# Kernel optimization log

Hardware: AMD Instinct MI355X
Metric: run time of the kernel (lower is better)

Reference implementation:

```python
import jax, jax.numpy as jnp
import numpy as np

PATCH = 3  # patch_size (init kwarg)
STRIDE = 1  # stride (init kwarg)
EPS_NORMALIZE = 1e-12  # F.normalize default eps
EPS_PATCH = 1e-5       # patch-norm eps in feature_match_index


def _unit_channels(feat):
    # F.normalize(feat.reshape(c,-1), dim=0): unit L2 norm over channels per pixel.
    n = jnp.linalg.norm(feat, axis=0, keepdims=True)
    return feat / jnp.maximum(n, EPS_NORMALIZE)


def _patches(feat, ps):
    # feat: (c, h, w) -> (c*ps*ps, n_patches) row-major over (h-ps+1, w-ps+1)
    c, h, w = feat.shape
    hp, wp = h - ps + 1, w - ps + 1
    cols = jnp.stack([feat[:, dy:dy + hp, dx:dx + wp]
                      for dy in range(ps) for dx in range(ps)], axis=1)  # (c, ps*ps, hp, wp)
    return cols.reshape(c * ps * ps, hp * wp)


def _per_item(fi, fr):
    # fi, fr: (c, h, w)
    c, h, w = fi.shape
    ps = PATCH
    hp, wp = h - ps + 1, w - ps + 1

    fi = _unit_channels(fi)
    fr = _unit_channels(fr)

    ref = _patches(fr, ps)                                   # (c*9, n_ref)
    ref = ref / (jnp.linalg.norm(ref, axis=0, keepdims=True) + EPS_PATCH)
    inp = _patches(fi, ps)                                   # (c*9, n_in)

    # Full cross-correlation cost volume (= chunked conv2d + running max in torch code)
    corr = jnp.einsum('ki,kr->ir', inp, ref)                 # (n_in, n_ref)
    max_idx = jnp.argmax(corr, axis=1).reshape(hp, wp)       # first occurrence on ties, same as torch running '>' max

    # index_to_flow
    flow_w = (max_idx % wp).astype(jnp.float32)
    flow_h = (max_idx // wp).astype(jnp.float32)
    grid_x = jnp.arange(wp, dtype=jnp.float32)[None, :]
    grid_y = jnp.arange(hp, dtype=jnp.float32)[:, None]
    flow = jnp.stack([flow_w - grid_x * jnp.ones((hp, wp), jnp.float32),
                      flow_h - grid_y * jnp.ones((hp, wp), jnp.float32)], axis=-1)  # (hp, wp, 2)
    flow = jnp.pad(flow, ((0, ps - 1), (0, ps - 1), (0, 0)))  # (h, w, 2)

    # tensor_shift for (i, j) in {0,1,2}^2, zero fill
    shifted = jnp.stack([jnp.pad(flow, ((i, 0), (j, 0), (0, 0)))[:h, :w]
                         for i in range(3) for j in range(3)], axis=0)  # (9, h, w, 2)
    return shifted


def setup_inputs() -> dict:
    key = jax.random.key(0)
    k1, k2 = jax.random.split(key)
    N, C, H, W = 2, 64, 96, 96
    return {
        'dense_features1': jax.random.normal(k1, (N, C, H, W), dtype=jnp.float32),
        'dense_features2': jax.random.normal(k2, (N, C, H, W), dtype=jnp.float32),
    }


def reference(dense_features1, dense_features2):
    shifted = jax.vmap(_per_item)(dense_features1, dense_features2)  # (N, 9, H, W, 2)
    N, _, H, W, _ = shifted.shape
    # pre_offset_reorder: even channels = flow_h (offset[...,1]), odd channels = flow_w (offset[...,0])
    out = jnp.stack([shifted[..., 1], shifted[..., 0]], axis=2).reshape(N, 18, H, W)
    return out
```

## Files before the change

kernel.cpp:

```cpp
#include <hip/hip_runtime.h>
#include <math.h>

static constexpr int NITEM = 2;
static constexpr int C = 64;
static constexpr int W = 96;
static constexpr int H = 96;
static constexpr int HW = H * W;
static constexpr int HP = 94;
static constexpr int NP = HP * HP;

static constexpr int PL = 8;
static constexpr int UNITS_PER_N = 1188;
static constexpr int NBLOCKS = 768;

typedef float f32x2 __attribute__((ext_vector_type(2)));

#if defined(__has_builtin) && __has_builtin(__builtin_elementwise_fma)
#define VFMA(q, a, b) (q) = __builtin_elementwise_fma((a), (b), (q))
#else
#define VFMA(q, a, b) do { (q).x = fmaf((a).x, (b).x, (q).x); \
                           (q).y = fmaf((a).y, (b).y, (q).y); } while (0)
#endif

__device__ __forceinline__ unsigned int fkey(float v) {
    unsigned int u = __float_as_uint(v);
    return (u & 0x80000000u) ? ~u : (u | 0x80000000u);
}

__global__ __launch_bounds__(256) void normalize_kernel(
    const float* __restrict__ f1, const float* __restrict__ f2,
    float2* __restrict__ fiP, float* __restrict__ frP, float* __restrict__ ssn)
{
    int t = blockIdx.x * 256 + threadIdx.x;
    const int perTensor = NITEM * HW;
    if (t >= 2 * perTensor) return;
    int which = t / perTensor;
    int p = t - which * perTensor;
    int n = p / HW;
    int pix = p - n * HW;
    const float* src = (which ? f2 : f1) + (size_t)n * C * HW + pix;
    float s = 0.f;
    #pragma unroll
    for (int c = 0; c < C; c++) {
        float v = src[c * HW];
        s = fmaf(v, v, s);
    }
    float norm = sqrtf(s);
    float scale = 1.0f / fmaxf(norm, 1e-12f);
    int y = pix / W, x = pix - y * W;
    if (which) {
        float* base = frP + ((size_t)n * H + y) * (C * W) + x;
        #pragma unroll
        for (int c = 0; c < C; c++)
            base[c * W] = src[c * HW] * scale;
        ssn[p] = s * scale * scale;
    } else {
        float2* base = fiP + ((size_t)n * H + y) * (32 * W) + x;
        #pragma unroll
        for (int c2 = 0; c2 < 32; c2++)
            base[c2 * W] = make_float2(src[(2 * c2) * HW] * scale,
                                       src[(2 * c2 + 1) * HW] * scale);
    }
}

__global__ __launch_bounds__(256) void refnorm_kernel(
    const float* __restrict__ ssn, float* __restrict__ invn)
{
    int t = blockIdx.x * 256 + threadIdx.x;
    if (t >= NITEM * NP) return;
    int n = t / NP;
    int r = t - n * NP;
    int yr = r / HP, xr = r - yr * HP;
    const float* s = ssn + n * HW;
    float acc = 0.f;
    #pragma unroll
    for (int dy = 0; dy < 3; dy++)
        #pragma unroll
        for (int dx = 0; dx < 3; dx++)
            acc += s[(yr + dy) * W + (xr + dx)];
    invn[t] = 1.0f / (sqrtf(acc) + 1e-5f);
}

__device__ __forceinline__ void stage_row(const void* gsrc, void* ldst, int lane, int wv)
{
#if defined(__has_builtin) && __has_builtin(__builtin_amdgcn_global_load_lds)
    const char* g = (const char*)gsrc;
    char* l = (char*)ldst;
    #pragma unroll
    for (int c = 0; c < 6; ++c) {
        const int off = wv * 6144 + c * 1024;
        __builtin_amdgcn_global_load_lds(
            (const __attribute__((address_space(1))) unsigned int*)(const void*)(g + off + lane * 16),
            (__attribute__((address_space(3))) unsigned int*)(void*)(l + off),
            16, 0, 0);
    }
#else
    const char* g = (const char*)gsrc;
    char* l = (char*)ldst;
    #pragma unroll
    for (int c = 0; c < 6; ++c) {
        const int off = wv * 6144 + c * 1024 + lane * 16;
        *(float4*)(l + off) = *(const float4*)(g + off);
    }
#endif
}

__global__ __launch_bounds__(256, 2) void corr_fused_kernel(
    const float2* __restrict__ fiP, const float* __restrict__ frP,
    const float* __restrict__ invn, unsigned long long* __restrict__ best,
    unsigned int* __restrict__ tick)
{
    __shared__ struct {
        f32x2 A[32][96];
        float B[64][96];
        float sh[3][2][100];
        int   sp;
    } sm;

    const int t = threadIdx.x;
    const int tu = t >> 4, tv = t & 15;
    const int lane = t & 63;
    const int quad = tu & 3;
    const int wv = t >> 6;
    const int u0 = 6 * tu, v0 = 6 * tv;
    const unsigned long long gmask = 0xFFFFull << (lane & 48);

    const int n = blockIdx.x & 1;

    const float2* fiPn = fiP + (size_t)n * H * (32 * W);
    const float* frPn = frP + (size_t)n * H * (C * W);
    const float* inv = invn + (size_t)n * NP;
    unsigned long long* bn = best + (size_t)n * NP;

    float pA[6][6], pB[6][6];

    for (;;) {
        if (t == 0) sm.sp = (int)atomicAdd(&tick[n * 16], 1u);
        __syncthreads();
        const int uj = sm.sp;
        if (uj >= UNITS_PER_N) break;

        int dy = 0, ya = 0, nb = 0;
        {
            int r = uj;
            for (int s = 0; s < 187; ++s) {
                int ady = (s + 1) >> 1;
                int nyi = 94 - ady;
                int q = (nyi + PL - 1) / PL;
                if (r < q) {
                    dy = (s & 1) ? -ady : ady;
                    ya = (dy < 0 ? -dy : 0) + r * PL;
                    nb = nyi - r * PL; if (nb > PL) nb = PL;
                    break;
                }
                r -= q;
            }
        }
        const int yb = ya + nb;

        stage_row(fiPn + (size_t)ya * (32 * W), &sm.A[0][0], lane, wv);
        stage_row(frPn + (size_t)(ya + dy) * (C * W), &sm.B[0][0], lane, wv);
        asm volatile("s_waitcnt vmcnt(0)" ::: "memory");
        __syncthreads();

        for (int y = ya; y <= yb + 1; ++y) {
            const bool doLd = (y <= yb);
            const bool doFin = (y >= ya + 2);
            const bool doA = (y > ya);
            const int yi = y - 2;
            const int yr = yi + dy;

            f32x2 q[6][3];
            #pragma unroll
            for (int i = 0; i < 6; ++i)
                #pragma unroll
                for (int p = 0; p < 3; ++p) q[i][p] = (f32x2)(0.f);

            #pragma unroll 2
            for (int c2 = 0; c2 < 32; ++c2) {
                const float4* ap = (const float4*)&sm.A[c2][u0];
                float4 A0 = ap[0], A1 = ap[1], A2 = ap[2];
                const f32x2* bpe = (const f32x2*)&sm.B[2 * c2][v0];
                const f32x2* bpo = (const f32x2*)&sm.B[2 * c2 + 1][v0];
                f32x2 be0 = bpe[0], be1 = bpe[1], be2 = bpe[2];
                f32x2 bo0 = bpo[0], bo1 = bpo[1], bo2 = bpo[2];
                f32x2 s0 = {A0.x, A0.x}, s1 = {A0.z, A0.z}, s2 = {A1.x, A1.x},
                      s3 = {A1.z, A1.z}, s4 = {A2.x, A2.x}, s5 = {A2.z, A2.z};
                VFMA(q[0][0], s0, be0); VFMA(q[0][1], s0, be1); VFMA(q[0][2], s0, be2);
                VFMA(q[1][0], s1, be0); VFMA(q[1][1], s1, be1); VFMA(q[1][2], s1, be2);
                VFMA(q[2][0], s2, be0); VFMA(q[2][1], s2, be1); VFMA(q[2][2], s2, be2);
                VFMA(q[3][0], s3, be0); VFMA(q[3][1], s3, be1); VFMA(q[3][2], s3, be2);
                VFMA(q[4][0], s4, be0); VFMA(q[4][1], s4, be1); VFMA(q[4][2], s4, be2);
                VFMA(q[5][0], s5, be0); VFMA(q[5][1], s5, be1); VFMA(q[5][2], s5, be2);
                f32x2 r0 = {A0.y, A0.y}, r1 = {A0.w, A0.w}, r2 = {A1.y, A1.y},
                      r3 = {A1.w, A1.w}, r4 = {A2.y, A2.y}, r5 = {A2.w, A2.w};
                VFMA(q[0][0], r0, bo0); VFMA(q[0][1], r0, bo1); VFMA(q[0][2], r0, bo2);
                VFMA(q[1][0], r1, bo0); VFMA(q[1][1], r1, bo1); VFMA(q[1][2], r1, bo2);
                VFMA(q[2][0], r2, bo0); VFMA(q[2][1], r2, bo1); VFMA(q[2][2], r2, bo2);
                VFMA(q[3][0], r3, bo0); VFMA(q[3][1], r3, bo1); VFMA(q[3][2], r3, bo2);
                VFMA(q[4][0], r4, bo0); VFMA(q[4][1], r4, bo1); VFMA(q[4][2], r4, bo2);
                VFMA(q[5][0], r5, bo0); VFMA(q[5][1], r5, bo1); VFMA(q[5][2], r5, bo2);
            }

            float acc[6][6];
            #pragma unroll
            for (int i = 0; i < 6; ++i)
                #pragma unroll
                for (int jj = 0; jj < 6; ++jj) acc[i][jj] = q[i][jj >> 1][jj & 1];

            if (quad == 0 && tu >= 4) {
                const int g = (tu >> 2) - 1;
                #pragma unroll
                for (int jj = 0; jj < 6; ++jj) {
                    sm.sh[g][0][v0 + jj] = acc[0][jj];
                    sm.sh[g][1][v0 + jj] = acc[1][jj];
                }
            }
            __syncthreads();

            if (doLd) {
                stage_row(fiPn + (size_t)(y + 1) * (32 * W), &sm.A[0][0], lane, wv);
                stage_row(frPn + (size_t)(y + 1 + dy) * (C * W), &sm.B[0][0], lane, wv);
            }

            float c6[6], c7[6];
            #pragma unroll
            for (int i = 0; i < 6; ++i) {
                c6[i] = __shfl_down(acc[i][0], 1);
                c7[i] = __shfl_down(acc[i][1], 1);
            }
            float e6[8], e7[8];
            #pragma unroll
            for (int jj = 0; jj < 6; ++jj) {
                e6[jj] = __shfl_down(acc[0][jj], 16);
                e7[jj] = __shfl_down(acc[1][jj], 16);
            }
            e6[6] = __shfl_down(acc[0][0], 17);
            e6[7] = __shfl_down(acc[0][1], 17);
            e7[6] = __shfl_down(acc[1][0], 17);
            e7[7] = __shfl_down(acc[1][1], 17);
            if (quad == 3) {
                if (tu < 15) {
                    const int g = tu >> 2;
                    #pragma unroll
                    for (int jj = 0; jj < 8; ++jj) {
                        e6[jj] = sm.sh[g][0][v0 + jj];
                        e7[jj] = sm.sh[g][1][v0 + jj];
                    }
                } else {
                    #pragma unroll
                    for (int jj = 0; jj < 8; ++jj) { e6[jj] = 0.f; e7[jj] = 0.f; }
                }
            }

            float ivr[6];
            if (doFin) {
                const float* ivp = inv + (size_t)yr * HP;
                #pragma unroll
                for (int jj = 0; jj < 6; ++jj) {
                    int xr = v0 + jj;
                    ivr[jj] = ivp[xr > 93 ? 93 : xr];
                }
            }

            #pragma unroll
            for (int i = 0; i < 6; ++i) {
                float bv = -INFINITY; int bxr = 0;
                #pragma unroll
                for (int jj = 0; jj < 6; ++jj) {
                    const int i1 = (i + 1 <= 5) ? i + 1 : 0;
                    const int j1 = (jj + 1 <= 5) ? jj + 1 : 0;
                    const int i2 = (i + 2 <= 5) ? i + 2 : 0;
                    const int j2 = (jj + 2 <= 5) ? jj + 2 : 0;
                    float E0 = acc[i][jj];
                    float E1 = (i + 1 <= 5)
                             ? ((jj + 1 <= 5) ? acc[i1][j1] : c6[i1])
                             : e6[jj + 1];
                    float E2 = (i + 2 <= 5)
                             ? ((jj + 2 <= 5) ? acc[i2][j2]
                                              : ((jj + 2 == 6) ? c6[i2] : c7[i2]))
                             : ((i + 2 == 6) ? e6[jj + 2] : e7[jj + 2]);
                    float bx = (E0 + E1) + E2;
                    if (doFin) {
                        float v = (pA[i][jj] + bx) * ivr[jj];
                        int xr = v0 + jj;
                        if (xr < HP && (u0 + i) < HP && v > bv) { bv = v; bxr = xr; }
                    }
                    if (doA) pA[i][jj] = pB[i][jj] + bx;
                    pB[i][jj] = bx;
                }
                if (doFin) {
                    float mx = bv;
                    #pragma unroll
                    for (int m = 1; m < 16; m <<= 1)
                        mx = fmaxf(mx, __shfl_xor(mx, m));
                    unsigned long long ball = __ballot(bv == mx) & gmask;
                    int srcl = __ffsll(ball) - 1;
                    int wxr = __shfl(bxr, srcl);
                    if (tv == 0 && (u0 + i) < HP) {
                        unsigned long long key =
                            ((unsigned long long)fkey(mx) << 32)
                          | (unsigned int)(~(unsigned int)(yr * HP + wxr));
                        const size_t off = (size_t)yi * HP + (u0 + i);
                        if (key > bn[off]) atomicMax(&bn[off], key);
                    }
                }
            }

            if (doLd) asm volatile("s_waitcnt vmcnt(0)" ::: "memory");
            __syncthreads();
        }
    }
}

__global__ __launch_bounds__(256) void expand_best_kernel(
    const unsigned long long* __restrict__ best, float* __restrict__ out)
{
    int t = blockIdx.x * 256 + threadIdx.x;
    const int total = NITEM * 18 * HW;
    if (t >= total) return;
    int x = t % W;
    int y = (t / W) % H;
    int chn = (t / HW) % 18;
    int n = t / (18 * HW);
    int k = chn >> 1;
    int b = chn & 1;
    int is = k / 3, js = k - is * 3;
    int ys = y - is, xs = x - js;
    float val = 0.f;
    if (ys >= 0 && ys < HP && xs >= 0 && xs < HP) {
        int i = ys * HP + xs;
        unsigned long long key = best[(size_t)n * NP + i];
        int idx = (int)(~(unsigned int)key);
        int yr = idx / HP, xr = idx - yr * HP;
        val = b ? (float)(xr - xs) : (float)(yr - ys);
    }
    out[t] = val;
}

extern "C" void kernel_launch(void* const* d_in, const int* in_sizes, int n_in,
                              void* d_out, int out_size, void* d_ws, size_t ws_size,
                              hipStream_t stream) {
    (void)in_sizes; (void)n_in; (void)out_size; (void)ws_size;
    const float* f1 = (const float*)d_in[0];
    const float* f2 = (const float*)d_in[1];

    float2* fiP = (float2*)d_ws;
    float*  frP = (float*)(fiP + (size_t)NITEM * H * 32 * W);
    float*  ssn = frP + (size_t)NITEM * H * C * W;
    float*  invn = ssn + (size_t)NITEM * HW;
    unsigned long long* best =
        (unsigned long long*)((((uintptr_t)(invn + (size_t)NITEM * NP)) + 63) & ~(uintptr_t)63);
    unsigned int* tick = (unsigned int*)(best + (size_t)NITEM * NP);

    normalize_kernel<<<(2 * NITEM * HW + 255) / 256, 256, 0, stream>>>(f1, f2, fiP, frP, ssn);
    refnorm_kernel<<<(NITEM * NP + 255) / 256, 256, 0, stream>>>(ssn, invn);
    hipMemsetAsync(best, 0, (size_t)NITEM * NP * sizeof(unsigned long long) + 512, stream);
    corr_fused_kernel<<<NBLOCKS, 256, 0, stream>>>(fiP, frP, invn, best, tick);
    expand_best_kernel<<<(NITEM * 18 * HW + 255) / 256, 256, 0, stream>>>(best, (float*)d_out);
}
```

Before: 564.1 us.

## Double-buffer half-row LDS staging to overlap loads with correlation FMAs

```diff
diff --git a/kernel.cpp b/kernel.cpp
--- a/kernel.cpp
+++ b/kernel.cpp
@@ -81,26 +81,25 @@
     invn[t] = 1.0f / (sqrtf(acc) + 1e-5f);
 }
 
-__device__ __forceinline__ void stage_row(const void* gsrc, void* ldst, int lane, int wv)
+__device__ __forceinline__ void stage_half(const char* aH, const char* bH,
+                                           char* slot, int wv, int lane)
 {
 #if defined(__has_builtin) && __has_builtin(__builtin_amdgcn_global_load_lds)
-    const char* g = (const char*)gsrc;
-    char* l = (char*)ldst;
     #pragma unroll
     for (int c = 0; c < 6; ++c) {
-        const int off = wv * 6144 + c * 1024;
+        const int off = (wv * 6 + c) << 10;
+        const char* g = ((off < 12288) ? (aH + off) : (bH + (off - 12288))) + lane * 16;
         __builtin_amdgcn_global_load_lds(
-            (const __attribute__((address_space(1))) unsigned int*)(const void*)(g + off + lane * 16),
-            (__attribute__((address_space(3))) unsigned int*)(void*)(l + off),
+            (const __attribute__((address_space(1))) unsigned int*)(const void*)g,
+            (__attribute__((address_space(3))) unsigned int*)(void*)(slot + off),
             16, 0, 0);
     }
 #else
-    const char* g = (const char*)gsrc;
-    char* l = (char*)ldst;
     #pragma unroll
     for (int c = 0; c < 6; ++c) {
-        const int off = wv * 6144 + c * 1024 + lane * 16;
-        *(float4*)(l + off) = *(const float4*)(g + off);
+        const int off = ((wv * 6 + c) << 10) + lane * 16;
+        const char* g = (off < 12288) ? (aH + off) : (bH + (off - 12288));
+        *(float4*)(slot + off) = *(const float4*)g;
     }
 #endif
 }
@@ -111,8 +110,7 @@
     unsigned int* __restrict__ tick)
 {
     __shared__ struct {
-        f32x2 A[32][96];
-        float B[64][96];
+        char  slot[2][24576];
         float sh[3][2][100];
         int   sp;
     } sm;
@@ -127,12 +125,13 @@
 
     const int n = blockIdx.x & 1;
 
-    const float2* fiPn = fiP + (size_t)n * H * (32 * W);
-    const float* frPn = frP + (size_t)n * H * (C * W);
+    const char* fiB = (const char*)(fiP + (size_t)n * H * (32 * W));
+    const char* frB = (const char*)(frP + (size_t)n * H * (C * W));
     const float* inv = invn + (size_t)n * NP;
     unsigned long long* bn = best + (size_t)n * NP;
 
     float pA[6][6], pB[6][6];
+    float acc[6][6];
 
     for (;;) {
         if (t == 0) sm.sp = (int)atomicAdd(&tick[n * 16], 1u);
@@ -156,72 +155,14 @@
                 r -= q;
             }
         }
-        const int yb = ya + nb;
-
-        stage_row(fiPn + (size_t)ya * (32 * W), &sm.A[0][0], lane, wv);
-        stage_row(frPn + (size_t)(ya + dy) * (C * W), &sm.B[0][0], lane, wv);
-        asm volatile("s_waitcnt vmcnt(0)" ::: "memory");
-        __syncthreads();
-
-        for (int y = ya; y <= yb + 1; ++y) {
-            const bool doLd = (y <= yb);
+        const int R = nb + 2;
+        const int K = 2 * R;
+
+        auto do_taps = [&](int y) {
             const bool doFin = (y >= ya + 2);
             const bool doA = (y > ya);
             const int yi = y - 2;
             const int yr = yi + dy;
-
-            f32x2 q[6][3];
-            #pragma unroll
-            for (int i = 0; i < 6; ++i)
-                #pragma unroll
-                for (int p = 0; p < 3; ++p) q[i][p] = (f32x2)(0.f);
-
-            #pragma unroll 2
-            for (int c2 = 0; c2 < 32; ++c2) {
-                const float4* ap = (const float4*)&sm.A[c2][u0];
-                float4 A0 = ap[0], A1 = ap[1], A2 = ap[2];
-                const f32x2* bpe = (const f32x2*)&sm.B[2 * c2][v0];
-                const f32x2* bpo = (const f32x2*)&sm.B[2 * c2 + 1][v0];
-                f32x2 be0 = bpe[0], be1 = bpe[1], be2 = bpe[2];
-                f32x2 bo0 = bpo[0], bo1 = bpo[1], bo2 = bpo[2];
-                f32x2 s0 = {A0.x, A0.x}, s1 = {A0.z, A0.z}, s2 = {A1.x, A1.x},
-                      s3 = {A1.z, A1.z}, s4 = {A2.x, A2.x}, s5 = {A2.z, A2.z};
-                VFMA(q[0][0], s0, be0); VFMA(q[0][1], s0, be1); VFMA(q[0][2], s0, be2);
-                VFMA(q[1][0], s1, be0); VFMA(q[1][1], s1, be1); VFMA(q[1][2], s1, be2);
-                VFMA(q[2][0], s2, be0); VFMA(q[2][1], s2, be1); VFMA(q[2][2], s2, be2);
-                VFMA(q[3][0], s3, be0); VFMA(q[3][1], s3, be1); VFMA(q[3][2], s3, be2);
-                VFMA(q[4][0], s4, be0); VFMA(q[4][1], s4, be1); VFMA(q[4][2], s4, be2);
-                VFMA(q[5][0], s5, be0); VFMA(q[5][1], s5, be1); VFMA(q[5][2], s5, be2);
-                f32x2 r0 = {A0.y, A0.y}, r1 = {A0.w, A0.w}, r2 = {A1.y, A1.y},
-                      r3 = {A1.w, A1.w}, r4 = {A2.y, A2.y}, r5 = {A2.w, A2.w};
-                VFMA(q[0][0], r0, bo0); VFMA(q[0][1], r0, bo1); VFMA(q[0][2], r0, bo2);
-                VFMA(q[1][0], r1, bo0); VFMA(q[1][1], r1, bo1); VFMA(q[1][2], r1, bo2);
-                VFMA(q[2][0], r2, bo0); VFMA(q[2][1], r2, bo1); VFMA(q[2][2], r2, bo2);
-                VFMA(q[3][0], r3, bo0); VFMA(q[3][1], r3, bo1); VFMA(q[3][2], r3, bo2);
-                VFMA(q[4][0], r4, bo0); VFMA(q[4][1], r4, bo1); VFMA(q[4][2], r4, bo2);
-                VFMA(q[5][0], r5, bo0); VFMA(q[5][1], r5, bo1); VFMA(q[5][2], r5, bo2);
-            }
-
-            float acc[6][6];
-            #pragma unroll
-            for (int i = 0; i < 6; ++i)
-                #pragma unroll
-                for (int jj = 0; jj < 6; ++jj) acc[i][jj] = q[i][jj >> 1][jj & 1];
-
-            if (quad == 0 && tu >= 4) {
-                const int g = (tu >> 2) - 1;
-                #pragma unroll
-                for (int jj = 0; jj < 6; ++jj) {
-                    sm.sh[g][0][v0 + jj] = acc[0][jj];
-                    sm.sh[g][1][v0 + jj] = acc[1][jj];
-                }
-            }
-            __syncthreads();
-
-            if (doLd) {
-                stage_row(fiPn + (size_t)(y + 1) * (32 * W), &sm.A[0][0], lane, wv);
-                stage_row(frPn + (size_t)(y + 1 + dy) * (C * W), &sm.B[0][0], lane, wv);
-            }
 
             float c6[6], c7[6];
             #pragma unroll
@@ -306,10 +247,86 @@
                     }
                 }
             }
-
-            if (doLd) asm volatile("s_waitcnt vmcnt(0)" ::: "memory");
-            __syncthreads();
+        };
+
+        stage_half(fiB + (size_t)ya * 24576,
+                   frB + (size_t)(ya + dy) * 24576,
+                   sm.slot[0], wv, lane);
+
+        f32x2 q[6][3];
+        for (int k = 0; k < K; ++k) {
+            const int r = k >> 1, h = k & 1;
+            const int y = ya + r;
+
+            __builtin_amdgcn_s_barrier();
+
+            if (k + 1 < K) {
+                const int k1 = k + 1, r1 = k1 >> 1, h1 = k1 & 1;
+                stage_half(fiB + (size_t)(ya + r1) * 24576 + h1 * 12288,
+                           frB + (size_t)(ya + r1 + dy) * 24576 + h1 * 12288,
+                           sm.slot[k1 & 1], wv, lane);
+            }
+
+            if (h == 0) {
+                if (r >= 1) do_taps(y - 1);
+                #pragma unroll
+                for (int i = 0; i < 6; ++i)
+                    #pragma unroll
+                    for (int p = 0; p < 3; ++p) q[i][p] = (f32x2)(0.f);
+            }
+
+            if (k + 1 < K) asm volatile("s_waitcnt vmcnt(6)" ::: "memory");
+            else           asm volatile("s_waitcnt vmcnt(0)" ::: "memory");
+
+            {
+                const char* base = sm.slot[k & 1];
+                #pragma unroll 2
+                for (int c2l = 0; c2l < 16; ++c2l) {
+                    const float4* ap = (const float4*)(base + c2l * 768 + u0 * 8);
+                    float4 A0 = ap[0], A1 = ap[1], A2 = ap[2];
+                    const float* brow = (const float*)(base + 12288);
+                    const f32x2* bpe = (const f32x2*)(brow + (2 * c2l) * 96 + v0);
+                    const f32x2* bpo = (const f32x2*)(brow + (2 * c2l + 1) * 96 + v0);
+                    f32x2 be0 = bpe[0], be1 = bpe[1], be2 = bpe[2];
+                    f32x2 bo0 = bpo[0], bo1 = bpo[1], bo2 = bpo[2];
+                    f32x2 s0 = {A0.x, A0.x}, s1 = {A0.z, A0.z}, s2 = {A1.x, A1.x},
+                          s3 = {A1.z, A1.z}, s4 = {A2.x, A2.x}, s5 = {A2.z, A2.z};
+                    VFMA(q[0][0], s0, be0); VFMA(q[0][1], s0, be1); VFMA(q[0][2], s0, be2);
+                    VFMA(q[1][0], s1, be0); VFMA(q[1][1], s1, be1); VFMA(q[1][2], s1, be2);
+                    VFMA(q[2][0], s2, be0); VFMA(q[2][1], s2, be1); VFMA(q[2][2], s2, be2);
+                    VFMA(q[3][0], s3, be0); VFMA(q[3][1], s3, be1); VFMA(q[3][2], s3, be2);
+                    VFMA(q[4][0], s4, be0); VFMA(q[4][1], s4, be1); VFMA(q[4][2], s4, be2);
+                    VFMA(q[5][0], s5, be0); VFMA(q[5][1], s5, be1); VFMA(q[5][2], s5, be2);
+                    f32x2 r0 = {A0.y, A0.y}, r1 = {A0.w, A0.w}, r2 = {A1.y, A1.y},
+                          r3 = {A1.w, A1.w}, r4 = {A2.y, A2.y}, r5 = {A2.w, A2.w};
+                    VFMA(q[0][0], r0, bo0); VFMA(q[0][1], r0, bo1); VFMA(q[0][2], r0, bo2);
+                    VFMA(q[1][0], r1, bo0); VFMA(q[1][1], r1, bo1); VFMA(q[1][2], r1, bo2);
+                    VFMA(q[2][0], r2, bo0); VFMA(q[2][1], r2, bo1); VFMA(q[2][2], r2, bo2);
+                    VFMA(q[3][0], r3, bo0); VFMA(q[3][1], r3, bo1); VFMA(q[3][2], r3, bo2);
+                    VFMA(q[4][0], r4, bo0); VFMA(q[4][1], r4, bo1); VFMA(q[4][2], r4, bo2);
+                    VFMA(q[5][0], r5, bo0); VFMA(q[5][1], r5, bo1); VFMA(q[5][2], r5, bo2);
+                }
+            }
+
+            if (h == 1) {
+                #pragma unroll
+                for (int i = 0; i < 6; ++i)
+                    #pragma unroll
+                    for (int jj = 0; jj < 6; ++jj) acc[i][jj] = q[i][jj >> 1][jj & 1];
+                if (quad == 0 && tu >= 4) {
+                    const int g = (tu >> 2) - 1;
+                    #pragma unroll
+                    for (int jj = 0; jj < 6; ++jj) {
+                        sm.sh[g][0][v0 + jj] = acc[0][jj];
+                        sm.sh[g][1][v0 + jj] = acc[1][jj];
+                    }
+                }
+                asm volatile("s_waitcnt lgkmcnt(0)" ::: "memory");
+            }
         }
+
+        __builtin_amdgcn_s_barrier();
+        do_taps(ya + R - 1);
     }
 }
 
```

Result: slower. 601.8 us (+6.7%).

## Pair two vertical displacements per block to share staged input rows

Applied to the files above, without the earlier changes.

```diff
diff --git a/kernel.cpp b/kernel.cpp
--- a/kernel.cpp
+++ b/kernel.cpp
@@ -10,8 +10,8 @@
 static constexpr int NP = HP * HP;
 
 static constexpr int PL = 8;
-static constexpr int UNITS_PER_N = 1188;
-static constexpr int NBLOCKS = 768;
+static constexpr int UNITS_PER_N = 600;
+static constexpr int NBLOCKS = 512;
 
 typedef float f32x2 __attribute__((ext_vector_type(2)));
 
@@ -81,44 +81,43 @@
     invn[t] = 1.0f / (sqrtf(acc) + 1e-5f);
 }
 
-__device__ __forceinline__ void stage_row(const void* gsrc, void* ldst, int lane, int wv)
-{
+__device__ __forceinline__ void stage_unit(const char* aRow, const char* b0Row,
+                                           const char* b1Row, char* smA,
+                                           char* smB0, char* smB1, int wv, int lane)
+{
+    #pragma unroll
+    for (int c = 0; c < 9; ++c) {
+        const int id = wv * 9 + c;
+        const char* g; char* d;
+        if (id < 24)      { g = aRow  + (id << 10);        d = smA  + (id << 10); }
+        else if (id < 48) { g = b0Row + ((id - 24) << 10); d = smB0 + ((id - 24) << 10); }
+        else              { g = b1Row + ((id - 48) << 10); d = smB1 + ((id - 48) << 10); }
 #if defined(__has_builtin) && __has_builtin(__builtin_amdgcn_global_load_lds)
-    const char* g = (const char*)gsrc;
-    char* l = (char*)ldst;
-    #pragma unroll
-    for (int c = 0; c < 6; ++c) {
-        const int off = wv * 6144 + c * 1024;
         __builtin_amdgcn_global_load_lds(
-            (const __attribute__((address_space(1))) unsigned int*)(const void*)(g + off + lane * 16),
-            (__attribute__((address_space(3))) unsigned int*)(void*)(l + off),
-            16, 0, 0);
-    }
+            (const __attribute__((address_space(1))) unsigned int*)(const void*)(g + lane * 16),
+            (__attribute__((address_space(3))) unsigned int*)(void*)d, 16, 0, 0);
 #else
-    const char* g = (const char*)gsrc;
-    char* l = (char*)ldst;
-    #pragma unroll
-    for (int c = 0; c < 6; ++c) {
-        const int off = wv * 6144 + c * 1024 + lane * 16;
-        *(float4*)(l + off) = *(const float4*)(g + off);
-    }
+        *(float4*)(d + lane * 16) = *(const float4*)(g + lane * 16);
 #endif
-}
-
-__global__ __launch_bounds__(256, 2) void corr_fused_kernel(
+    }
+}
+
+__global__ __launch_bounds__(512, 2) void corr_fused_kernel(
     const float2* __restrict__ fiP, const float* __restrict__ frP,
     const float* __restrict__ invn, unsigned long long* __restrict__ best,
     unsigned int* __restrict__ tick)
 {
     __shared__ struct {
         f32x2 A[32][96];
-        float B[64][96];
-        float sh[3][2][100];
+        float B[2][64][96];
+        float sh[2][3][2][100];
         int   sp;
     } sm;
 
     const int t = threadIdx.x;
-    const int tu = t >> 4, tv = t & 15;
+    const int half = t >> 8;
+    const int tl = t & 255;
+    const int tu = tl >> 4, tv = tl & 15;
     const int lane = t & 63;
     const int quad = tu & 3;
     const int wv = t >> 6;
@@ -127,8 +126,8 @@
 
     const int n = blockIdx.x & 1;
 
-    const float2* fiPn = fiP + (size_t)n * H * (32 * W);
-    const float* frPn = frP + (size_t)n * H * (C * W);
+    const char* fiB = (const char*)(fiP + (size_t)n * H * (32 * W));
+    const char* frB = (const char*)(frP + (size_t)n * H * (C * W));
     const float* inv = invn + (size_t)n * NP;
     unsigned long long* bn = best + (size_t)n * NP;
 
@@ -140,35 +139,46 @@
         const int uj = sm.sp;
         if (uj >= UNITS_PER_N) break;
 
-        int dy = 0, ya = 0, nb = 0;
+        int s = 0, ya = 0, nb = 0;
         {
             int r = uj;
-            for (int s = 0; s < 187; ++s) {
-                int ady = (s + 1) >> 1;
-                int nyi = 94 - ady;
-                int q = (nyi + PL - 1) / PL;
+            for (s = 0; s < 94; ++s) {
+                int nyi0 = 94 - s;
+                int q = (nyi0 + PL - 1) / PL;
                 if (r < q) {
-                    dy = (s & 1) ? -ady : ady;
-                    ya = (dy < 0 ? -dy : 0) + r * PL;
-                    nb = nyi - r * PL; if (nb > PL) nb = PL;
+                    ya = ((s & 1) ? s : 0) + r * PL;
+                    nb = nyi0 - r * PL; if (nb > PL) nb = PL;
                     break;
                 }
                 r -= q;
             }
         }
+        const int sgn = (s & 1) ? -1 : 1;
+        const int d0 = sgn * s;
+        const int d1 = sgn * (s + 1);
+        const int dyh = half ? d1 : d0;
+        const int yloH = half ? ((s & 1) ? s + 1 : 0) : ((s & 1) ? s : 0);
+        const int yhiH = yloH + (half ? (93 - s) : (94 - s));
         const int yb = ya + nb;
 
-        stage_row(fiPn + (size_t)ya * (32 * W), &sm.A[0][0], lane, wv);
-        stage_row(frPn + (size_t)(ya + dy) * (C * W), &sm.B[0][0], lane, wv);
+        {
+            int r0 = ya + d0; r0 = r0 < 0 ? 0 : (r0 > 95 ? 95 : r0);
+            int r1 = ya + d1; r1 = r1 < 0 ? 0 : (r1 > 95 ? 95 : r1);
+            stage_unit(fiB + (size_t)ya * 24576, frB + (size_t)r0 * 24576,
+                       frB + (size_t)r1 * 24576, (char*)&sm.A[0][0],
+                       (char*)&sm.B[0][0][0], (char*)&sm.B[1][0][0], wv, lane);
+        }
         asm volatile("s_waitcnt vmcnt(0)" ::: "memory");
         __syncthreads();
 
+        const float (*smB)[96] = sm.B[half];
+
         for (int y = ya; y <= yb + 1; ++y) {
             const bool doLd = (y <= yb);
-            const bool doFin = (y >= ya + 2);
+            const int yi = y - 2;
+            const bool doFin = (y >= ya + 2) && (yi >= yloH) && (yi < yhiH);
             const bool doA = (y > ya);
-            const int yi = y - 2;
-            const int yr = yi + dy;
+            const int yr = yi + dyh;
 
             f32x2 q[6][3];
             #pragma unroll
@@ -180,8 +190,8 @@
             for (int c2 = 0; c2 < 32; ++c2) {
                 const float4* ap = (const float4*)&sm.A[c2][u0];
                 float4 A0 = ap[0], A1 = ap[1], A2 = ap[2];
-                const f32x2* bpe = (const f32x2*)&sm.B[2 * c2][v0];
-                const f32x2* bpo = (const f32x2*)&sm.B[2 * c2 + 1][v0];
+                const f32x2* bpe = (const f32x2*)&smB[2 * c2][v0];
+                const f32x2* bpo = (const f32x2*)&smB[2 * c2 + 1][v0];
                 f32x2 be0 = bpe[0], be1 = bpe[1], be2 = bpe[2];
                 f32x2 bo0 = bpo[0], bo1 = bpo[1], bo2 = bpo[2];
                 f32x2 s0 = {A0.x, A0.x}, s1 = {A0.z, A0.z}, s2 = {A1.x, A1.x},
@@ -212,15 +222,18 @@
                 const int g = (tu >> 2) - 1;
                 #pragma unroll
                 for (int jj = 0; jj < 6; ++jj) {
-                    sm.sh[g][0][v0 + jj] = acc[0][jj];
-                    sm.sh[g][1][v0 + jj] = acc[1][jj];
+                    sm.sh[half][g][0][v0 + jj] = acc[0][jj];
+                    sm.sh[half][g][1][v0 + jj] = acc[1][jj];
                 }
             }
             __syncthreads();
 
             if (doLd) {
-                stage_row(fiPn + (size_t)(y + 1) * (32 * W), &sm.A[0][0], lane, wv);
-                stage_row(frPn + (size_t)(y + 1 + dy) * (C * W), &sm.B[0][0], lane, wv);
+                int r0 = y + 1 + d0; r0 = r0 < 0 ? 0 : (r0 > 95 ? 95 : r0);
+                int r1 = y + 1 + d1; r1 = r1 < 0 ? 0 : (r1 > 95 ? 95 : r1);
+                stage_unit(fiB + (size_t)(y + 1) * 24576, frB + (size_t)r0 * 24576,
+                           frB + (size_t)r1 * 24576, (char*)&sm.A[0][0],
+                           (char*)&sm.B[0][0][0], (char*)&sm.B[1][0][0], wv, lane);
             }
 
             float c6[6], c7[6];
@@ -244,8 +257,8 @@
                     const int g = tu >> 2;
                     #pragma unroll
                     for (int jj = 0; jj < 8; ++jj) {
-                        e6[jj] = sm.sh[g][0][v0 + jj];
-                        e7[jj] = sm.sh[g][1][v0 + jj];
+                        e6[jj] = sm.sh[half][g][0][v0 + jj];
+                        e7[jj] = sm.sh[half][g][1][v0 + jj];
                     }
                 } else {
                     #pragma unroll
@@ -356,6 +369,6 @@
     normalize_kernel<<<(2 * NITEM * HW + 255) / 256, 256, 0, stream>>>(f1, f2, fiP, frP, ssn);
     refnorm_kernel<<<(NITEM * NP + 255) / 256, 256, 0, stream>>>(ssn, invn);
     hipMemsetAsync(best, 0, (size_t)NITEM * NP * sizeof(unsigned long long) + 512, stream);
-    corr_fused_kernel<<<NBLOCKS, 256, 0, stream>>>(fiP, frP, invn, best, tick);
+    corr_fused_kernel<<<NBLOCKS, 512, 0, stream>>>(fiP, frP, invn, best, tick);
     expand_best_kernel<<<(NITEM * 18 * HW + 255) / 256, 256, 0, stream>>>(best, (float*)d_out);
 }
```

Measured after the change: 618.2 us. +9.6%, slower.
